# Kernel tuning notes

Hardware: AMD Instinct MI355X
Metric: run time of the kernel (lower is better)

Reference implementation:

```python
import jax, jax.numpy as jnp
import numpy as np
from jax import lax

H = 100  # hidden size (hardcoded in the module)


def _lstm_cell(x, h, c, W_ih, W_hh, b):
    # gates: [B, 4H] in PyTorch order i, f, g, o
    gates = x @ W_ih.T + h @ W_hh.T + b
    i, f, g, o = jnp.split(gates, 4, axis=-1)
    c = jax.nn.sigmoid(f) * c + jax.nn.sigmoid(i) * jnp.tanh(g)
    h = jax.nn.sigmoid(o) * jnp.tanh(c)
    return h, c


def setup_inputs() -> dict:
    key = jax.random.key(0)
    ks = jax.random.split(key, 12)
    B, T = 512, 1000
    s = 0.1  # keep gates away from saturation
    return {
        "input": jax.random.normal(ks[0], (B, T), dtype=jnp.float32),
        "W_ih1": jax.random.normal(ks[1], (4 * H, 1), dtype=jnp.float32) * s,
        "W_hh1": jax.random.normal(ks[2], (4 * H, H), dtype=jnp.float32) * s,
        "b_ih1": jax.random.normal(ks[3], (4 * H,), dtype=jnp.float32) * s,
        "b_hh1": jax.random.normal(ks[4], (4 * H,), dtype=jnp.float32) * s,
        "W_ih2": jax.random.normal(ks[5], (4 * H, H), dtype=jnp.float32) * s,
        "W_hh2": jax.random.normal(ks[6], (4 * H, H), dtype=jnp.float32) * s,
        "b_ih2": jax.random.normal(ks[7], (4 * H,), dtype=jnp.float32) * s,
        "b_hh2": jax.random.normal(ks[8], (4 * H,), dtype=jnp.float32) * s,
        "W_lin": jax.random.normal(ks[9], (1, H), dtype=jnp.float32) * s,
        "b_lin": jax.random.normal(ks[10], (1,), dtype=jnp.float32) * s,
        "future": 300,
    }


def reference(input, W_ih1, W_hh1, b_ih1, b_hh1, W_ih2, W_hh2, b_ih2, b_hh2,
              W_lin, b_lin, future):
    B = input.shape[0]
    b1 = b_ih1 + b_hh1
    b2 = b_ih2 + b_hh2
    xs = input.T[:, :, None]  # [T, B, 1]
    z = jnp.zeros((B, H), dtype=input.dtype)

    def step(carry, x):
        h1, c1, h2, c2 = carry
        h1, c1 = _lstm_cell(x, h1, c1, W_ih1, W_hh1, b1)
        h2, c2 = _lstm_cell(h1, h2, c2, W_ih2, W_hh2, b2)
        y = h2 @ W_lin.T + b_lin  # [B, 1]
        return (h1, c1, h2, c2), y

    carry, ys = lax.scan(step, (z, z, z, z), xs)  # ys: [T, B, 1]

    def fstep(carry, _):
        h1, c1, h2, c2, y = carry
        h1, c1 = _lstm_cell(y, h1, c1, W_ih1, W_hh1, b1)
        h2, c2 = _lstm_cell(h1, h2, c2, W_ih2, W_hh2, b2)
        y = h2 @ W_lin.T + b_lin
        return (h1, c1, h2, c2, y), y

    h1, c1, h2, c2 = carry
    _, ys_f = lax.scan(fstep, (h1, c1, h2, c2, ys[-1]), None, length=future)

    out = jnp.concatenate([ys, ys_f], axis=0)  # [T+future, B, 1]
    return out[:, :, 0].T  # [B, T+future]
```

## Files before the change

kernel.cpp:

```cpp
#include <hip/hip_runtime.h>
#include <stdint.h>

#define HID 100
#define B_TOTAL 512
#define T_IN 1000
#define NB 2
#define BLOCK 512
#define RSTR 160

typedef __fp16 f16x8 __attribute__((ext_vector_type(8)));
typedef __fp16 f16x2 __attribute__((ext_vector_type(2)));
typedef float f32x4 __attribute__((ext_vector_type(4)));

#define MF(A, B, C) __builtin_amdgcn_mfma_f32_16x16x32_f16((A), (B), (C), 0, 0, 0)
#define Z4 ((f32x4){0.f, 0.f, 0.f, 0.f})

#if __has_builtin(__builtin_amdgcn_exp2f)
#define EXP2F(x) __builtin_amdgcn_exp2f(x)
#else
#define EXP2F(x) exp2f(x)
#endif
#if __has_builtin(__builtin_amdgcn_rcpf)
#define RCPF(x) __builtin_amdgcn_rcpf(x)
#else
#define RCPF(x) (1.0f / (x))
#endif
#define LOG2E 1.44269504f
__device__ __forceinline__ float sigm(float x) { return RCPF(1.0f + EXP2F(-LOG2E * x)); }
__device__ __forceinline__ float tanh_fast(float x) {
  return 1.0f - 2.0f * RCPF(EXP2F((2.0f * LOG2E) * x) + 1.0f);
}

__device__ __forceinline__ float dot8(f16x8 a, f16x8 b, float acc) {
#if __has_builtin(__builtin_amdgcn_fdot2)
#pragma unroll
  for (int q = 0; q < 4; q++) {
    f16x2 xa = {a[2 * q], a[2 * q + 1]};
    f16x2 xb = {b[2 * q], b[2 * q + 1]};
    acc = __builtin_amdgcn_fdot2(xa, xb, acc, false);
  }
#else
#pragma unroll
  for (int e = 0; e < 8; e++) acc = fmaf((float)a[e], (float)b[e], acc);
#endif
  return acc;
}

__device__ __forceinline__ int jmap(int tl, int m) { return (m & 3) * 100 + 4 * tl + (m >> 2); }

__device__ __forceinline__ __fp16 w1e(const float* Whh1, const float* Wih1,
                                      const float* bih1, const float* bhh1, int j, int k) {
  if (k < 100) return (__fp16)Whh1[j * 100 + k];
  if (k == 100) return (__fp16)Wih1[j];
  if (k == 101 || k == 102) {
    float b = bih1[j] + bhh1[j];
    __fp16 hi = (__fp16)b;
    return (k == 101) ? hi : (__fp16)(b - (float)hi);
  }
  return (__fp16)0.0f;
}
__device__ __forceinline__ __fp16 w2e(const float* Wih2, const float* Whh2,
                                      const float* bih2, const float* bhh2, int j, int k) {
  if (k < 100) return (__fp16)Wih2[j * 100 + k];
  if (k == 101 || k == 102) {
    float b = bih2[j] + bhh2[j];
    __fp16 hi = (__fp16)b;
    return (k == 101) ? hi : (__fp16)(b - (float)hi);
  }
  if (k >= 112 && k < 212) return (__fp16)Whh2[j * 100 + (k - 112)];
  return (__fp16)0.0f;
}

__device__ __forceinline__ f16x8 mka1(const float* Whh1, const float* Wih1,
                                      const float* bih1, const float* bhh1,
                                      int tl, int kt, int m, int kg) {
  int j = jmap(tl, m);
  f16x8 r;
#pragma unroll
  for (int e = 0; e < 8; e++) r[e] = w1e(Whh1, Wih1, bih1, bhh1, j, kt * 32 + kg * 8 + e);
  return r;
}
__device__ __forceinline__ f16x8 mka2(const float* Wih2, const float* Whh2,
                                      const float* bih2, const float* bhh2,
                                      int tl, int kt, int m, int kg) {
  int j = jmap(tl, m);
  f16x8 r;
#pragma unroll
  for (int e = 0; e < 8; e++) r[e] = w2e(Wih2, Whh2, bih2, bhh2, j, kt * 32 + kg * 8 + e);
  return r;
}

__global__ __launch_bounds__(BLOCK, 2) void lstm2_mfma(
    const float* __restrict__ input,
    const float* __restrict__ Wih1,
    const float* __restrict__ Whh1,
    const float* __restrict__ bih1,
    const float* __restrict__ bhh1,
    const float* __restrict__ Wih2,
    const float* __restrict__ Whh2,
    const float* __restrict__ bih2,
    const float* __restrict__ bhh2,
    const float* __restrict__ Wlin,
    const float* __restrict__ blin,
    const int* __restrict__ futp,
    float* __restrict__ out)
{
  __shared__ __align__(16) __fp16 H1X[2][NB][RSTR];
  __shared__ __align__(16) __fp16 H2s[2][NB][RSTR];
  __shared__ __align__(16) float  ybuf[2][NB][104];
  __shared__ __align__(16) float  xrow[NB][T_IN];
  __shared__ __align__(16) __fp16 T24[11 * 64 * 8];
  __shared__ float wls[104];

  const int tid = threadIdx.x;
  const int lane = tid & 63;
  const int wv = tid >> 6;
  const int b0 = blockIdx.x * NB;
  const int F = futp[0];
  const int TT = T_IN + F;

  for (int i = tid; i < NB * T_IN; i += BLOCK) {
    int b = i / T_IN, tt = i % T_IN;
    xrow[b][tt] = input[(size_t)(b0 + b) * T_IN + tt];
  }
  { uint32_t* z = (uint32_t*)H1X; if (tid < 320) z[tid] = 0u; }
  { uint32_t* z = (uint32_t*)H2s; if (tid < 320) z[tid] = 0u; }
  { float* z = (float*)ybuf; if (tid < 416) z[tid] = 0.0f; }
  if (tid < 104) wls[tid] = (tid < HID) ? Wlin[tid] : 0.0f;

  const int n15 = lane & 15;
  const int kg = lane >> 4;
  const int bcol = lane & 1;

  const int sel = lane & 15;
  const int cg  = sel >> 1;
  const int ab  = sel & 1;
  const int aq  = lane >> 4;
  const int atl = (cg == 0) ? wv : (cg == 1) ? 8 + wv : (cg == 2) ? 16 + wv : 24;
  const int ak  = atl * 4 + aq;
  const bool awr1 = (sel < 6) || (wv == 0 && sel < 8);
  const bool awr2 = (sel < 6) || (wv == 1 && sel < 8);
  float c1v = 0.0f, c2v = 0.0f;

  const int is_y = (tid >= 496);
  const int ybat = ((tid - 496) >> 3) & 1;
  const int yl = (tid - 496) & 7;
  const float blin0 = blin[0];

  f16x8 wlinv[4];
#pragma unroll
  for (int i = 0; i < 4; i++) {
#pragma unroll
    for (int e = 0; e < 8; e++) {
      int k = i * 32 + kg * 8 + e;
      wlinv[i][e] = (__fp16)((k < HID) ? Wlin[k] : 0.f);
    }
  }
  f32x4 wih1q;
#pragma unroll
  for (int g = 0; g < 4; g++) wih1q[g] = Wih1[g * 100 + ak];

  f16x8 W1f0[4], W1f1[4], W1f2[4], W2f0[7], W2f1[7], W2f2[7];
#pragma unroll
  for (int kt = 0; kt < 4; kt++) {
    W1f0[kt] = mka1(Whh1, Wih1, bih1, bhh1, wv, kt, n15, kg);
    W1f1[kt] = mka1(Whh1, Wih1, bih1, bhh1, 8 + wv, kt, n15, kg);
    W1f2[kt] = mka1(Whh1, Wih1, bih1, bhh1, 16 + wv, kt, n15, kg);
  }
#pragma unroll
  for (int kt = 0; kt < 7; kt++) {
    W2f0[kt] = mka2(Wih2, Whh2, bih2, bhh2, wv, kt, n15, kg);
    W2f1[kt] = mka2(Wih2, Whh2, bih2, bhh2, 8 + wv, kt, n15, kg);
    W2f2[kt] = mka2(Wih2, Whh2, bih2, bhh2, 16 + wv, kt, n15, kg);
  }
  if (tid < 64) {
    f16x8* TV = (f16x8*)T24;
    const int m_ = tid & 15, kg_ = tid >> 4;
#pragma unroll
    for (int kt = 0; kt < 4; kt++) TV[kt * 64 + tid] = mka1(Whh1, Wih1, bih1, bhh1, 24, kt, m_, kg_);
#pragma unroll
    for (int kt = 0; kt < 3; kt++) TV[(4 + kt) * 64 + tid] = mka2(Wih2, Whh2, bih2, bhh2, 24, 4 + kt, m_, kg_);
#pragma unroll
    for (int kt = 0; kt < 4; kt++) TV[(7 + kt) * 64 + tid] = mka2(Wih2, Whh2, bih2, bhh2, 24, kt, m_, kg_);
  }

  __syncthreads();
  if (tid < 4) { H1X[tid >> 1][tid & 1][101] = (__fp16)1.0f; H1X[tid >> 1][tid & 1][102] = (__fp16)1.0f; }
  if (tid >= 4 && tid < 6) H1X[1][tid - 4][100] = (__fp16)xrow[tid - 4][0];
  __syncthreads();

  f16x8 bH1a[4], bH2[3], bl2m;
  f32x4 c0, c1, c2, c3, d0, d1, d2, d3;

#define RD_H1A(P) { _Pragma("unroll") for (int kt_ = 0; kt_ < 4; kt_++) \
    bH1a[kt_] = *(const f16x8*)&H1X[P][bcol][kt_ * 32 + kg * 8]; }
#define RD_L2M(P) { f16x8 hm_ = *(const f16x8*)&H2s[P][bcol][(kg >= 2) ? ((kg - 2) * 8) : 0]; \
    bl2m = (kg >= 2) ? hm_ : bH1a[3]; }
#define RD_H2P(P) { _Pragma("unroll") for (int kt_ = 0; kt_ < 3; kt_++) \
    bH2[kt_] = *(const f16x8*)&H2s[P][bcol][16 + kt_ * 32 + kg * 8]; }

#define MFMA_L1 { \
    c0 = Z4; c1 = Z4; c2 = Z4; c3 = Z4; \
    _Pragma("unroll") for (int kt_ = 0; kt_ < 4; kt_++) { \
      c0 = MF(W1f0[kt_], bH1a[kt_], c0); c1 = MF(W1f1[kt_], bH1a[kt_], c1); c2 = MF(W1f2[kt_], bH1a[kt_], c2); } \
    if (wv == 0) { const f16x8* TV = (const f16x8*)T24; \
      _Pragma("unroll") for (int kt_ = 0; kt_ < 4; kt_++) c3 = MF(TV[kt_ * 64 + lane], bH1a[kt_], c3); } }

#define MFMA_L2 { \
    d0 = Z4; d1 = Z4; d2 = Z4; d3 = Z4; \
    _Pragma("unroll") for (int kt_ = 0; kt_ < 3; kt_++) { \
      d0 = MF(W2f0[kt_], bH1a[kt_], d0); d1 = MF(W2f1[kt_], bH1a[kt_], d1); d2 = MF(W2f2[kt_], bH1a[kt_], d2); } \
    d0 = MF(W2f0[3], bl2m, d0); d1 = MF(W2f1[3], bl2m, d1); d2 = MF(W2f2[3], bl2m, d2); \
    _Pragma("unroll") for (int kt_ = 0; kt_ < 3; kt_++) { \
      d0 = MF(W2f0[kt_ + 4], bH2[kt_], d0); d1 = MF(W2f1[kt_ + 4], bH2[kt_], d1); d2 = MF(W2f2[kt_ + 4], bH2[kt_], d2); } \
    if (wv == 1) { const f16x8* TV = (const f16x8*)T24; \
      _Pragma("unroll") for (int kt_ = 0; kt_ < 3; kt_++) d3 = MF(TV[(7 + kt_) * 64 + lane], bH1a[kt_], d3); \
      d3 = MF(TV[10 * 64 + lane], bl2m, d3); \
      _Pragma("unroll") for (int kt_ = 0; kt_ < 3; kt_++) d3 = MF(TV[(4 + kt_) * 64 + lane], bH2[kt_], d3); } }

#define ACT1_TF(W_) { \
    f32x4 qq = (cg == 0) ? c0 : (cg == 1) ? c1 : (cg == 2) ? c2 : c3; \
    float sf_ = sigm(qq[1]), si_ = sigm(qq[0]), tg_ = tanh_fast(qq[2]); \
    c1v = sf_ * c1v + si_ * tg_; \
    float h_ = sigm(qq[3]) * tanh_fast(c1v); \
    if (awr1) H1X[W_][ab][ak] = (__fp16)h_; }

#define ACT1_AR(W_, YV_) { \
    f32x4 qq = (cg == 0) ? c0 : (cg == 1) ? c1 : (cg == 2) ? c2 : c3; \
    qq[0] = fmaf(wih1q[0], (YV_), qq[0]); qq[1] = fmaf(wih1q[1], (YV_), qq[1]); \
    qq[2] = fmaf(wih1q[2], (YV_), qq[2]); qq[3] = fmaf(wih1q[3], (YV_), qq[3]); \
    float sf_ = sigm(qq[1]), si_ = sigm(qq[0]), tg_ = tanh_fast(qq[2]); \
    c1v = sf_ * c1v + si_ * tg_; \
    float h_ = sigm(qq[3]) * tanh_fast(c1v); \
    if (awr1) H1X[W_][ab][ak] = (__fp16)h_; }

#define ACT2(W_, YB_) { \
    f32x4 qq = (cg == 0) ? d0 : (cg == 1) ? d1 : (cg == 2) ? d2 : d3; \
    float sf_ = sigm(qq[1]), si_ = sigm(qq[0]), tg_ = tanh_fast(qq[2]); \
    c2v = sf_ * c2v + si_ * tg_; \
    float h_ = sigm(qq[3]) * tanh_fast(c2v); \
    if (awr2) { H2s[W_][ab][ak] = (__fp16)h_; if (YB_) ybuf[W_][ab][ak] = h_; } }

#define Y_BODY(tt, RP) { \
    const float* yb_ = &ybuf[RP][ybat][0]; \
    float s = 0.0f; \
    _Pragma("unroll") \
    for (int m = 0; m < 13; m++) s = fmaf(yb_[yl + 8 * m], wls[yl + 8 * m], s); \
    s += __shfl_down(s, 4, 8); \
    s += __shfl_down(s, 2, 8); \
    s += __shfl_down(s, 1, 8); \
    if (yl == 0) out[(size_t)(b0 + ybat) * TT + (tt)] = s + blin0; }

  RD_H1A(1)
  MFMA_L1
  ACT1_TF(0)
  if (tid >= 80 && tid < 82) H1X[0][tid - 80][100] = (__fp16)xrow[tid - 80][1];
  __syncthreads();

  for (int t = 0; t < T_IN - 1; t++) {
    const int p = t & 1, w = p ^ 1;
    RD_H1A(p) RD_L2M(p) RD_H2P(p)
    MFMA_L2
    MFMA_L1
    if (is_y && t > 0) Y_BODY(t - 1, p)
    if (tid >= 80 && tid < 82 && t + 2 < T_IN)
      H1X[w][tid - 80][100] = (__fp16)xrow[tid - 80][t + 2];
    ACT2(w, 1)
    ACT1_TF(w)
    __syncthreads();
  }

  if (kg == 0) {
    W1f0[3][4] = (__fp16)0.f; W1f1[3][4] = (__fp16)0.f; W1f2[3][4] = (__fp16)0.f;
  }
  if (tid < 16) ((__fp16*)T24)[3 * 512 + tid * 8 + 4] = (__fp16)0.f;
  __syncthreads();

  for (int t = T_IN - 1; t < TT; t++) {
    const int p = t & 1, w = p ^ 1;
    RD_H1A(p) RD_L2M(p) RD_H2P(p)
    MFMA_L2
    MFMA_L1
    if (is_y && t == T_IN - 1) Y_BODY(t - 1, p)
    ACT2(w, 0)
    __syncthreads();
    float s_ = 0.f;
#pragma unroll
    for (int i_ = 0; i_ < 4; i_++) {
      f16x8 hh_ = *(const f16x8*)&H2s[w][bcol][i_ * 32 + kg * 8];
      s_ = dot8(hh_, wlinv[i_], s_);
    }
    s_ += __shfl_xor(s_, 16, 64);
    s_ += __shfl_xor(s_, 32, 64);
    const float yv = s_ + blin0;
    if (wv == 0 && lane < 2) out[(size_t)(b0 + lane) * TT + t] = yv;
    ACT1_AR(w, yv)
    __syncthreads();
  }
}

extern "C" void kernel_launch(void* const* d_in, const int* in_sizes, int n_in,
                              void* d_out, int out_size, void* d_ws, size_t ws_size,
                              hipStream_t stream) {
  const float* input = (const float*)d_in[0];
  const float* Wih1  = (const float*)d_in[1];
  const float* Whh1  = (const float*)d_in[2];
  const float* bih1  = (const float*)d_in[3];
  const float* bhh1  = (const float*)d_in[4];
  const float* Wih2  = (const float*)d_in[5];
  const float* Whh2  = (const float*)d_in[6];
  const float* bih2  = (const float*)d_in[7];
  const float* bhh2  = (const float*)d_in[8];
  const float* Wlin  = (const float*)d_in[9];
  const float* blin  = (const float*)d_in[10];
  const int*   futp  = (const int*)d_in[11];
  float* out = (float*)d_out;

  dim3 grid(B_TOTAL / NB);
  dim3 block(BLOCK);
  hipLaunchKernelGGL(lstm2_mfma, grid, block, 0, stream,
                     input, Wih1, Whh1, bih1, bhh1, Wih2, Whh2, bih2, bhh2,
                     Wlin, blin, futp, out);
}
```

Before: 1.576 ms.

## Halve block to four waves with all weights in registers and fused output reduction

The block shrinks from 8 waves to 4, and each wave now holds seven gate tiles of weight fragments in registers. This removes the LDS-resident T24 tile that was used for the 25th tile. The linear output projection is computed in ACT2 with a wave shuffle reduction into a small partials buffer, replacing the dedicated Y threads and the dot8 path. The aim is lower barrier cost and fewer LDS reads per step, at the price of more serial MFMA work per wave and much higher register pressure with occupancy 1.

```diff
diff --git a/kernel.cpp b/kernel.cpp
--- a/kernel.cpp
+++ b/kernel.cpp
@@ -5,15 +5,15 @@
 #define B_TOTAL 512
 #define T_IN 1000
 #define NB 2
-#define BLOCK 512
+#define BLOCK 256
 #define RSTR 160
 
 typedef __fp16 f16x8 __attribute__((ext_vector_type(8)));
-typedef __fp16 f16x2 __attribute__((ext_vector_type(2)));
 typedef float f32x4 __attribute__((ext_vector_type(4)));
 
 #define MF(A, B, C) __builtin_amdgcn_mfma_f32_16x16x32_f16((A), (B), (C), 0, 0, 0)
 #define Z4 ((f32x4){0.f, 0.f, 0.f, 0.f})
+#define ZH8 ((f16x8){(__fp16)0.f,(__fp16)0.f,(__fp16)0.f,(__fp16)0.f,(__fp16)0.f,(__fp16)0.f,(__fp16)0.f,(__fp16)0.f})
 
 #if __has_builtin(__builtin_amdgcn_exp2f)
 #define EXP2F(x) __builtin_amdgcn_exp2f(x)
@@ -31,21 +31,6 @@
   return 1.0f - 2.0f * RCPF(EXP2F((2.0f * LOG2E) * x) + 1.0f);
 }
 
-__device__ __forceinline__ float dot8(f16x8 a, f16x8 b, float acc) {
-#if __has_builtin(__builtin_amdgcn_fdot2)
-#pragma unroll
-  for (int q = 0; q < 4; q++) {
-    f16x2 xa = {a[2 * q], a[2 * q + 1]};
-    f16x2 xb = {b[2 * q], b[2 * q + 1]};
-    acc = __builtin_amdgcn_fdot2(xa, xb, acc, false);
-  }
-#else
-#pragma unroll
-  for (int e = 0; e < 8; e++) acc = fmaf((float)a[e], (float)b[e], acc);
-#endif
-  return acc;
-}
-
 __device__ __forceinline__ int jmap(int tl, int m) { return (m & 3) * 100 + 4 * tl + (m >> 2); }
 
 __device__ __forceinline__ __fp16 w1e(const float* Whh1, const float* Wih1,
@@ -90,7 +75,7 @@
   return r;
 }
 
-__global__ __launch_bounds__(BLOCK, 2) void lstm2_mfma(
+__global__ __launch_bounds__(BLOCK, 1) void lstm2_mfma(
     const float* __restrict__ input,
     const float* __restrict__ Wih1,
     const float* __restrict__ Whh1,
@@ -107,10 +92,8 @@
 {
   __shared__ __align__(16) __fp16 H1X[2][NB][RSTR];
   __shared__ __align__(16) __fp16 H2s[2][NB][RSTR];
-  __shared__ __align__(16) float  ybuf[2][NB][104];
   __shared__ __align__(16) float  xrow[NB][T_IN];
-  __shared__ __align__(16) __fp16 T24[11 * 64 * 8];
-  __shared__ float wls[104];
+  __shared__ __align__(16) float  partials[2][NB][4];
 
   const int tid = threadIdx.x;
   const int lane = tid & 63;
@@ -123,10 +106,11 @@
     int b = i / T_IN, tt = i % T_IN;
     xrow[b][tt] = input[(size_t)(b0 + b) * T_IN + tt];
   }
-  { uint32_t* z = (uint32_t*)H1X; if (tid < 320) z[tid] = 0u; }
-  { uint32_t* z = (uint32_t*)H2s; if (tid < 320) z[tid] = 0u; }
-  { float* z = (float*)ybuf; if (tid < 416) z[tid] = 0.0f; }
-  if (tid < 104) wls[tid] = (tid < HID) ? Wlin[tid] : 0.0f;
+  for (int i = tid; i < 320; i += BLOCK) {
+    ((uint32_t*)H1X)[i] = 0u;
+    ((uint32_t*)H2s)[i] = 0u;
+  }
+  if (tid < 16) ((float*)partials)[tid] = 0.0f;
 
   const int n15 = lane & 15;
   const int kg = lane >> 4;
@@ -136,52 +120,34 @@
   const int cg  = sel >> 1;
   const int ab  = sel & 1;
   const int aq  = lane >> 4;
-  const int atl = (cg == 0) ? wv : (cg == 1) ? 8 + wv : (cg == 2) ? 16 + wv : 24;
-  const int ak  = atl * 4 + aq;
-  const bool awr1 = (sel < 6) || (wv == 0 && sel < 8);
-  const bool awr2 = (sel < 6) || (wv == 1 && sel < 8);
+  const bool actv = (cg < 6) || (wv == 3 && cg == 6);
+  const int ak = actv ? ((cg == 6) ? (96 + aq) : (16 * cg + 4 * wv + aq)) : 0;
   float c1v = 0.0f, c2v = 0.0f;
-
-  const int is_y = (tid >= 496);
-  const int ybat = ((tid - 496) >> 3) & 1;
-  const int yl = (tid - 496) & 7;
   const float blin0 = blin[0];
-
-  f16x8 wlinv[4];
-#pragma unroll
-  for (int i = 0; i < 4; i++) {
-#pragma unroll
-    for (int e = 0; e < 8; e++) {
-      int k = i * 32 + kg * 8 + e;
-      wlinv[i][e] = (__fp16)((k < HID) ? Wlin[k] : 0.f);
-    }
-  }
+  const float wlsv = Wlin[ak];
   f32x4 wih1q;
 #pragma unroll
   for (int g = 0; g < 4; g++) wih1q[g] = Wih1[g * 100 + ak];
 
-  f16x8 W1f0[4], W1f1[4], W1f2[4], W2f0[7], W2f1[7], W2f2[7];
-#pragma unroll
-  for (int kt = 0; kt < 4; kt++) {
-    W1f0[kt] = mka1(Whh1, Wih1, bih1, bhh1, wv, kt, n15, kg);
-    W1f1[kt] = mka1(Whh1, Wih1, bih1, bhh1, 8 + wv, kt, n15, kg);
-    W1f2[kt] = mka1(Whh1, Wih1, bih1, bhh1, 16 + wv, kt, n15, kg);
-  }
-#pragma unroll
-  for (int kt = 0; kt < 7; kt++) {
-    W2f0[kt] = mka2(Wih2, Whh2, bih2, bhh2, wv, kt, n15, kg);
-    W2f1[kt] = mka2(Wih2, Whh2, bih2, bhh2, 8 + wv, kt, n15, kg);
-    W2f2[kt] = mka2(Wih2, Whh2, bih2, bhh2, 16 + wv, kt, n15, kg);
-  }
-  if (tid < 64) {
-    f16x8* TV = (f16x8*)T24;
-    const int m_ = tid & 15, kg_ = tid >> 4;
-#pragma unroll
-    for (int kt = 0; kt < 4; kt++) TV[kt * 64 + tid] = mka1(Whh1, Wih1, bih1, bhh1, 24, kt, m_, kg_);
-#pragma unroll
-    for (int kt = 0; kt < 3; kt++) TV[(4 + kt) * 64 + tid] = mka2(Wih2, Whh2, bih2, bhh2, 24, 4 + kt, m_, kg_);
-#pragma unroll
-    for (int kt = 0; kt < 4; kt++) TV[(7 + kt) * 64 + tid] = mka2(Wih2, Whh2, bih2, bhh2, 24, kt, m_, kg_);
+  f16x8 W1f[7][4], W2f[7][7];
+#pragma unroll
+  for (int j = 0; j < 6; j++) {
+    const int tl_ = 4 * j + wv;
+#pragma unroll
+    for (int kt = 0; kt < 4; kt++) W1f[j][kt] = mka1(Whh1, Wih1, bih1, bhh1, tl_, kt, n15, kg);
+#pragma unroll
+    for (int kt = 0; kt < 7; kt++) W2f[j][kt] = mka2(Wih2, Whh2, bih2, bhh2, tl_, kt, n15, kg);
+  }
+  if (wv == 3) {
+#pragma unroll
+    for (int kt = 0; kt < 4; kt++) W1f[6][kt] = mka1(Whh1, Wih1, bih1, bhh1, 24, kt, n15, kg);
+#pragma unroll
+    for (int kt = 0; kt < 7; kt++) W2f[6][kt] = mka2(Wih2, Whh2, bih2, bhh2, 24, kt, n15, kg);
+  } else {
+#pragma unroll
+    for (int kt = 0; kt < 4; kt++) W1f[6][kt] = ZH8;
+#pragma unroll
+    for (int kt = 0; kt < 7; kt++) W2f[6][kt] = ZH8;
   }
 
   __syncthreads();
@@ -190,7 +156,7 @@
   __syncthreads();
 
   f16x8 bH1a[4], bH2[3], bl2m;
-  f32x4 c0, c1, c2, c3, d0, d1, d2, d3;
+  f32x4 dA[7], cA[7];
 
 #define RD_H1A(P) { _Pragma("unroll") for (int kt_ = 0; kt_ < 4; kt_++) \
     bH1a[kt_] = *(const f16x8*)&H1X[P][bcol][kt_ * 32 + kg * 8]; }
@@ -199,57 +165,47 @@
 #define RD_H2P(P) { _Pragma("unroll") for (int kt_ = 0; kt_ < 3; kt_++) \
     bH2[kt_] = *(const f16x8*)&H2s[P][bcol][16 + kt_ * 32 + kg * 8]; }
 
-#define MFMA_L1 { \
-    c0 = Z4; c1 = Z4; c2 = Z4; c3 = Z4; \
-    _Pragma("unroll") for (int kt_ = 0; kt_ < 4; kt_++) { \
-      c0 = MF(W1f0[kt_], bH1a[kt_], c0); c1 = MF(W1f1[kt_], bH1a[kt_], c1); c2 = MF(W1f2[kt_], bH1a[kt_], c2); } \
-    if (wv == 0) { const f16x8* TV = (const f16x8*)T24; \
-      _Pragma("unroll") for (int kt_ = 0; kt_ < 4; kt_++) c3 = MF(TV[kt_ * 64 + lane], bH1a[kt_], c3); } }
-
-#define MFMA_L2 { \
-    d0 = Z4; d1 = Z4; d2 = Z4; d3 = Z4; \
-    _Pragma("unroll") for (int kt_ = 0; kt_ < 3; kt_++) { \
-      d0 = MF(W2f0[kt_], bH1a[kt_], d0); d1 = MF(W2f1[kt_], bH1a[kt_], d1); d2 = MF(W2f2[kt_], bH1a[kt_], d2); } \
-    d0 = MF(W2f0[3], bl2m, d0); d1 = MF(W2f1[3], bl2m, d1); d2 = MF(W2f2[3], bl2m, d2); \
-    _Pragma("unroll") for (int kt_ = 0; kt_ < 3; kt_++) { \
-      d0 = MF(W2f0[kt_ + 4], bH2[kt_], d0); d1 = MF(W2f1[kt_ + 4], bH2[kt_], d1); d2 = MF(W2f2[kt_ + 4], bH2[kt_], d2); } \
-    if (wv == 1) { const f16x8* TV = (const f16x8*)T24; \
-      _Pragma("unroll") for (int kt_ = 0; kt_ < 3; kt_++) d3 = MF(TV[(7 + kt_) * 64 + lane], bH1a[kt_], d3); \
-      d3 = MF(TV[10 * 64 + lane], bl2m, d3); \
-      _Pragma("unroll") for (int kt_ = 0; kt_ < 3; kt_++) d3 = MF(TV[(4 + kt_) * 64 + lane], bH2[kt_], d3); } }
-
-#define ACT1_TF(W_) { \
-    f32x4 qq = (cg == 0) ? c0 : (cg == 1) ? c1 : (cg == 2) ? c2 : c3; \
+#define MFMA_L2 { _Pragma("unroll") for (int j = 0; j < 7; j++) { f32x4 a_ = Z4; \
+    a_ = MF(W2f[j][0], bH1a[0], a_); a_ = MF(W2f[j][1], bH1a[1], a_); a_ = MF(W2f[j][2], bH1a[2], a_); \
+    a_ = MF(W2f[j][3], bl2m, a_); \
+    a_ = MF(W2f[j][4], bH2[0], a_); a_ = MF(W2f[j][5], bH2[1], a_); a_ = MF(W2f[j][6], bH2[2], a_); \
+    dA[j] = a_; } }
+
+#define MFMA_L1 { _Pragma("unroll") for (int j = 0; j < 7; j++) { f32x4 a_ = Z4; \
+    a_ = MF(W1f[j][0], bH1a[0], a_); a_ = MF(W1f[j][1], bH1a[1], a_); \
+    a_ = MF(W1f[j][2], bH1a[2], a_); a_ = MF(W1f[j][3], bH1a[3], a_); \
+    cA[j] = a_; } }
+
+#define SELD (cg==0?dA[0]:cg==1?dA[1]:cg==2?dA[2]:cg==3?dA[3]:cg==4?dA[4]:cg==5?dA[5]:dA[6])
+#define SELC (cg==0?cA[0]:cg==1?cA[1]:cg==2?cA[2]:cg==3?cA[3]:cg==4?cA[4]:cg==5?cA[5]:cA[6])
+
+#define ACT2(W_, PW_) { f32x4 qq = SELD; \
+    float sf_ = sigm(qq[1]), si_ = sigm(qq[0]), tg_ = tanh_fast(qq[2]); \
+    c2v = sf_ * c2v + si_ * tg_; \
+    float h_ = sigm(qq[3]) * tanh_fast(c2v); \
+    if (actv) H2s[W_][ab][ak] = (__fp16)h_; \
+    float pc_ = actv ? h_ * wlsv : 0.0f; \
+    pc_ += __shfl_xor(pc_, 2, 64);  pc_ += __shfl_xor(pc_, 4, 64); \
+    pc_ += __shfl_xor(pc_, 8, 64);  pc_ += __shfl_xor(pc_, 16, 64); \
+    pc_ += __shfl_xor(pc_, 32, 64); \
+    if (lane < 2) partials[PW_][lane][wv] = pc_; }
+
+#define ACT1_TF(W_) { f32x4 qq = SELC; \
     float sf_ = sigm(qq[1]), si_ = sigm(qq[0]), tg_ = tanh_fast(qq[2]); \
     c1v = sf_ * c1v + si_ * tg_; \
     float h_ = sigm(qq[3]) * tanh_fast(c1v); \
-    if (awr1) H1X[W_][ab][ak] = (__fp16)h_; }
-
-#define ACT1_AR(W_, YV_) { \
-    f32x4 qq = (cg == 0) ? c0 : (cg == 1) ? c1 : (cg == 2) ? c2 : c3; \
+    if (actv) H1X[W_][ab][ak] = (__fp16)h_; }
+
+#define ACT1_AR(W_, YV_) { f32x4 qq = SELC; \
     qq[0] = fmaf(wih1q[0], (YV_), qq[0]); qq[1] = fmaf(wih1q[1], (YV_), qq[1]); \
     qq[2] = fmaf(wih1q[2], (YV_), qq[2]); qq[3] = fmaf(wih1q[3], (YV_), qq[3]); \
     float sf_ = sigm(qq[1]), si_ = sigm(qq[0]), tg_ = tanh_fast(qq[2]); \
     c1v = sf_ * c1v + si_ * tg_; \
     float h_ = sigm(qq[3]) * tanh_fast(c1v); \
-    if (awr1) H1X[W_][ab][ak] = (__fp16)h_; }
-
-#define ACT2(W_, YB_) { \
-    f32x4 qq = (cg == 0) ? d0 : (cg == 1) ? d1 : (cg == 2) ? d2 : d3; \
-    float sf_ = sigm(qq[1]), si_ = sigm(qq[0]), tg_ = tanh_fast(qq[2]); \
-    c2v = sf_ * c2v + si_ * tg_; \
-    float h_ = sigm(qq[3]) * tanh_fast(c2v); \
-    if (awr2) { H2s[W_][ab][ak] = (__fp16)h_; if (YB_) ybuf[W_][ab][ak] = h_; } }
-
-#define Y_BODY(tt, RP) { \
-    const float* yb_ = &ybuf[RP][ybat][0]; \
-    float s = 0.0f; \
-    _Pragma("unroll") \
-    for (int m = 0; m < 13; m++) s = fmaf(yb_[yl + 8 * m], wls[yl + 8 * m], s); \
-    s += __shfl_down(s, 4, 8); \
-    s += __shfl_down(s, 2, 8); \
-    s += __shfl_down(s, 1, 8); \
-    if (yl == 0) out[(size_t)(b0 + ybat) * TT + (tt)] = s + blin0; }
+    if (actv) H1X[W_][ab][ak] = (__fp16)h_; }
+
+#define YSUM(PP_, DST_) { const f32x4 pv_ = *(const f32x4*)&partials[PP_][ab][0]; \
+    DST_ = pv_[0] + pv_[1] + pv_[2] + pv_[3] + blin0; }
 
   RD_H1A(1)
   MFMA_L1
@@ -261,38 +217,38 @@
     const int p = t & 1, w = p ^ 1;
     RD_H1A(p) RD_L2M(p) RD_H2P(p)
     MFMA_L2
+    ACT2(w, p)
     MFMA_L1
-    if (is_y && t > 0) Y_BODY(t - 1, p)
+    if (wv == 0 && lane < 2 && t > 0) {
+      float yv_;
+      YSUM(p ^ 1, yv_)
+      out[(size_t)(b0 + lane) * TT + (t - 1)] = yv_;
+    }
     if (tid >= 80 && tid < 82 && t + 2 < T_IN)
       H1X[w][tid - 80][100] = (__fp16)xrow[tid - 80][t + 2];
-    ACT2(w, 1)
     ACT1_TF(w)
     __syncthreads();
   }
 
   if (kg == 0) {
-    W1f0[3][4] = (__fp16)0.f; W1f1[3][4] = (__fp16)0.f; W1f2[3][4] = (__fp16)0.f;
-  }
-  if (tid < 16) ((__fp16*)T24)[3 * 512 + tid * 8 + 4] = (__fp16)0.f;
-  __syncthreads();
+#pragma unroll
+    for (int j = 0; j < 7; j++) W1f[j][3][4] = (__fp16)0.f;
+  }
 
   for (int t = T_IN - 1; t < TT; t++) {
     const int p = t & 1, w = p ^ 1;
     RD_H1A(p) RD_L2M(p) RD_H2P(p)
     MFMA_L2
+    if (t == T_IN - 1 && wv == 0 && lane < 2) {
+      float yv_;
+      YSUM(p ^ 1, yv_)
+      out[(size_t)(b0 + lane) * TT + (t - 1)] = yv_;
+    }
+    ACT2(w, p)
     MFMA_L1
-    if (is_y && t == T_IN - 1) Y_BODY(t - 1, p)
-    ACT2(w, 0)
     __syncthreads();
-    float s_ = 0.f;
-#pragma unroll
-    for (int i_ = 0; i_ < 4; i_++) {
-      f16x8 hh_ = *(const f16x8*)&H2s[w][bcol][i_ * 32 + kg * 8];
-      s_ = dot8(hh_, wlinv[i_], s_);
-    }
-    s_ += __shfl_xor(s_, 16, 64);
-    s_ += __shfl_xor(s_, 32, 64);
-    const float yv = s_ + blin0;
+    float yv;
+    YSUM(p, yv)
     if (wv == 0 && lane < 2) out[(size_t)(b0 + lane) * TT + t] = yv;
     ACT1_AR(w, yv)
     __syncthreads();
```

New measurement: 2.242 ms. 1.42x slower.

## Keep tail gate weights in registers and compute teacher-forced output via wave 7 dot

Applied to the files above, without the earlier changes.

Moves the 25th-tile weight fragments for both layers from shared memory (T24) into per-wave registers on waves 0 and 1, so the MFMA loops no longer issue LDS reads for them. The float ybuf/wls path for the linear head is replaced by wave 7 computing the output from the fp16 H2s state with packed dot8 and two shuffles. ACT2 is moved before the layer-1 MFMAs to interleave transcendental work with matrix ops. The x-input writer threads move to another wave. This raises VGPR pressure, which could spill or lower occupancy under launch_bounds(512,2), and the head now reads fp16 rather than fp32 h2 in the teacher-forced phase.

```diff
diff --git a/kernel.cpp b/kernel.cpp
--- a/kernel.cpp
+++ b/kernel.cpp
@@ -14,6 +14,7 @@
 
 #define MF(A, B, C) __builtin_amdgcn_mfma_f32_16x16x32_f16((A), (B), (C), 0, 0, 0)
 #define Z4 ((f32x4){0.f, 0.f, 0.f, 0.f})
+#define ZH8 ((f16x8){(__fp16)0.f,(__fp16)0.f,(__fp16)0.f,(__fp16)0.f,(__fp16)0.f,(__fp16)0.f,(__fp16)0.f,(__fp16)0.f})
 
 #if __has_builtin(__builtin_amdgcn_exp2f)
 #define EXP2F(x) __builtin_amdgcn_exp2f(x)
@@ -107,10 +108,7 @@
 {
   __shared__ __align__(16) __fp16 H1X[2][NB][RSTR];
   __shared__ __align__(16) __fp16 H2s[2][NB][RSTR];
-  __shared__ __align__(16) float  ybuf[2][NB][104];
   __shared__ __align__(16) float  xrow[NB][T_IN];
-  __shared__ __align__(16) __fp16 T24[11 * 64 * 8];
-  __shared__ float wls[104];
 
   const int tid = threadIdx.x;
   const int lane = tid & 63;
@@ -123,10 +121,7 @@
     int b = i / T_IN, tt = i % T_IN;
     xrow[b][tt] = input[(size_t)(b0 + b) * T_IN + tt];
   }
-  { uint32_t* z = (uint32_t*)H1X; if (tid < 320) z[tid] = 0u; }
-  { uint32_t* z = (uint32_t*)H2s; if (tid < 320) z[tid] = 0u; }
-  { float* z = (float*)ybuf; if (tid < 416) z[tid] = 0.0f; }
-  if (tid < 104) wls[tid] = (tid < HID) ? Wlin[tid] : 0.0f;
+  if (tid < 320) { ((uint32_t*)H1X)[tid] = 0u; ((uint32_t*)H2s)[tid] = 0u; }
 
   const int n15 = lane & 15;
   const int kg = lane >> 4;
@@ -141,10 +136,6 @@
   const bool awr1 = (sel < 6) || (wv == 0 && sel < 8);
   const bool awr2 = (sel < 6) || (wv == 1 && sel < 8);
   float c1v = 0.0f, c2v = 0.0f;
-
-  const int is_y = (tid >= 496);
-  const int ybat = ((tid - 496) >> 3) & 1;
-  const int yl = (tid - 496) & 7;
   const float blin0 = blin[0];
 
   f16x8 wlinv[4];
@@ -173,15 +164,18 @@
     W2f1[kt] = mka2(Wih2, Whh2, bih2, bhh2, 8 + wv, kt, n15, kg);
     W2f2[kt] = mka2(Wih2, Whh2, bih2, bhh2, 16 + wv, kt, n15, kg);
   }
-  if (tid < 64) {
-    f16x8* TV = (f16x8*)T24;
-    const int m_ = tid & 15, kg_ = tid >> 4;
-#pragma unroll
-    for (int kt = 0; kt < 4; kt++) TV[kt * 64 + tid] = mka1(Whh1, Wih1, bih1, bhh1, 24, kt, m_, kg_);
-#pragma unroll
-    for (int kt = 0; kt < 3; kt++) TV[(4 + kt) * 64 + tid] = mka2(Wih2, Whh2, bih2, bhh2, 24, 4 + kt, m_, kg_);
-#pragma unroll
-    for (int kt = 0; kt < 4; kt++) TV[(7 + kt) * 64 + tid] = mka2(Wih2, Whh2, bih2, bhh2, 24, kt, m_, kg_);
+  f16x8 W1T[4], W2T[7];
+#pragma unroll
+  for (int kt = 0; kt < 4; kt++) W1T[kt] = ZH8;
+#pragma unroll
+  for (int kt = 0; kt < 7; kt++) W2T[kt] = ZH8;
+  if (wv == 0) {
+#pragma unroll
+    for (int kt = 0; kt < 4; kt++) W1T[kt] = mka1(Whh1, Wih1, bih1, bhh1, 24, kt, n15, kg);
+  }
+  if (wv == 1) {
+#pragma unroll
+    for (int kt = 0; kt < 7; kt++) W2T[kt] = mka2(Wih2, Whh2, bih2, bhh2, 24, kt, n15, kg);
   }
 
   __syncthreads();
@@ -190,7 +184,9 @@
   __syncthreads();
 
   f16x8 bH1a[4], bH2[3], bl2m;
-  f32x4 c0, c1, c2, c3, d0, d1, d2, d3;
+  f32x4 c0, c1, c2, d0, d1, d2;
+  f32x4 c3 = Z4, d3 = Z4;
+  const f32x4 zz = Z4;
 
 #define RD_H1A(P) { _Pragma("unroll") for (int kt_ = 0; kt_ < 4; kt_++) \
     bH1a[kt_] = *(const f16x8*)&H1X[P][bcol][kt_ * 32 + kg * 8]; }
@@ -199,24 +195,27 @@
 #define RD_H2P(P) { _Pragma("unroll") for (int kt_ = 0; kt_ < 3; kt_++) \
     bH2[kt_] = *(const f16x8*)&H2s[P][bcol][16 + kt_ * 32 + kg * 8]; }
 
+#define MFMA_L2 { \
+    d0 = MF(W2f0[0], bH1a[0], zz); d1 = MF(W2f1[0], bH1a[0], zz); d2 = MF(W2f2[0], bH1a[0], zz); \
+    d0 = MF(W2f0[1], bH1a[1], d0); d1 = MF(W2f1[1], bH1a[1], d1); d2 = MF(W2f2[1], bH1a[1], d2); \
+    d0 = MF(W2f0[2], bH1a[2], d0); d1 = MF(W2f1[2], bH1a[2], d1); d2 = MF(W2f2[2], bH1a[2], d2); \
+    d0 = MF(W2f0[3], bl2m, d0);    d1 = MF(W2f1[3], bl2m, d1);    d2 = MF(W2f2[3], bl2m, d2); \
+    d0 = MF(W2f0[4], bH2[0], d0);  d1 = MF(W2f1[4], bH2[0], d1);  d2 = MF(W2f2[4], bH2[0], d2); \
+    d0 = MF(W2f0[5], bH2[1], d0);  d1 = MF(W2f1[5], bH2[1], d1);  d2 = MF(W2f2[5], bH2[1], d2); \
+    d0 = MF(W2f0[6], bH2[2], d0);  d1 = MF(W2f1[6], bH2[2], d1);  d2 = MF(W2f2[6], bH2[2], d2); \
+    if (wv == 1) { \
+      d3 = MF(W2T[0], bH1a[0], zz); d3 = MF(W2T[1], bH1a[1], d3); d3 = MF(W2T[2], bH1a[2], d3); \
+      d3 = MF(W2T[3], bl2m, d3); \
+      d3 = MF(W2T[4], bH2[0], d3);  d3 = MF(W2T[5], bH2[1], d3);  d3 = MF(W2T[6], bH2[2], d3); } }
+
 #define MFMA_L1 { \
-    c0 = Z4; c1 = Z4; c2 = Z4; c3 = Z4; \
-    _Pragma("unroll") for (int kt_ = 0; kt_ < 4; kt_++) { \
-      c0 = MF(W1f0[kt_], bH1a[kt_], c0); c1 = MF(W1f1[kt_], bH1a[kt_], c1); c2 = MF(W1f2[kt_], bH1a[kt_], c2); } \
-    if (wv == 0) { const f16x8* TV = (const f16x8*)T24; \
-      _Pragma("unroll") for (int kt_ = 0; kt_ < 4; kt_++) c3 = MF(TV[kt_ * 64 + lane], bH1a[kt_], c3); } }
-
-#define MFMA_L2 { \
-    d0 = Z4; d1 = Z4; d2 = Z4; d3 = Z4; \
-    _Pragma("unroll") for (int kt_ = 0; kt_ < 3; kt_++) { \
-      d0 = MF(W2f0[kt_], bH1a[kt_], d0); d1 = MF(W2f1[kt_], bH1a[kt_], d1); d2 = MF(W2f2[kt_], bH1a[kt_], d2); } \
-    d0 = MF(W2f0[3], bl2m, d0); d1 = MF(W2f1[3], bl2m, d1); d2 = MF(W2f2[3], bl2m, d2); \
-    _Pragma("unroll") for (int kt_ = 0; kt_ < 3; kt_++) { \
-      d0 = MF(W2f0[kt_ + 4], bH2[kt_], d0); d1 = MF(W2f1[kt_ + 4], bH2[kt_], d1); d2 = MF(W2f2[kt_ + 4], bH2[kt_], d2); } \
-    if (wv == 1) { const f16x8* TV = (const f16x8*)T24; \
-      _Pragma("unroll") for (int kt_ = 0; kt_ < 3; kt_++) d3 = MF(TV[(7 + kt_) * 64 + lane], bH1a[kt_], d3); \
-      d3 = MF(TV[10 * 64 + lane], bl2m, d3); \
-      _Pragma("unroll") for (int kt_ = 0; kt_ < 3; kt_++) d3 = MF(TV[(4 + kt_) * 64 + lane], bH2[kt_], d3); } }
+    c0 = MF(W1f0[0], bH1a[0], zz); c1 = MF(W1f1[0], bH1a[0], zz); c2 = MF(W1f2[0], bH1a[0], zz); \
+    c0 = MF(W1f0[1], bH1a[1], c0); c1 = MF(W1f1[1], bH1a[1], c1); c2 = MF(W1f2[1], bH1a[1], c2); \
+    c0 = MF(W1f0[2], bH1a[2], c0); c1 = MF(W1f1[2], bH1a[2], c1); c2 = MF(W1f2[2], bH1a[2], c2); \
+    c0 = MF(W1f0[3], bH1a[3], c0); c1 = MF(W1f1[3], bH1a[3], c1); c2 = MF(W1f2[3], bH1a[3], c2); \
+    if (wv == 0) { \
+      c3 = MF(W1T[0], bH1a[0], zz); c3 = MF(W1T[1], bH1a[1], c3); \
+      c3 = MF(W1T[2], bH1a[2], c3); c3 = MF(W1T[3], bH1a[3], c3); } }
 
 #define ACT1_TF(W_) { \
     f32x4 qq = (cg == 0) ? c0 : (cg == 1) ? c1 : (cg == 2) ? c2 : c3; \
@@ -234,55 +233,53 @@
     float h_ = sigm(qq[3]) * tanh_fast(c1v); \
     if (awr1) H1X[W_][ab][ak] = (__fp16)h_; }
 
-#define ACT2(W_, YB_) { \
+#define ACT2(W_) { \
     f32x4 qq = (cg == 0) ? d0 : (cg == 1) ? d1 : (cg == 2) ? d2 : d3; \
     float sf_ = sigm(qq[1]), si_ = sigm(qq[0]), tg_ = tanh_fast(qq[2]); \
     c2v = sf_ * c2v + si_ * tg_; \
     float h_ = sigm(qq[3]) * tanh_fast(c2v); \
-    if (awr2) { H2s[W_][ab][ak] = (__fp16)h_; if (YB_) ybuf[W_][ab][ak] = h_; } }
-
-#define Y_BODY(tt, RP) { \
-    const float* yb_ = &ybuf[RP][ybat][0]; \
-    float s = 0.0f; \
-    _Pragma("unroll") \
-    for (int m = 0; m < 13; m++) s = fmaf(yb_[yl + 8 * m], wls[yl + 8 * m], s); \
-    s += __shfl_down(s, 4, 8); \
-    s += __shfl_down(s, 2, 8); \
-    s += __shfl_down(s, 1, 8); \
-    if (yl == 0) out[(size_t)(b0 + ybat) * TT + (tt)] = s + blin0; }
+    if (awr2) H2s[W_][ab][ak] = (__fp16)h_; }
+
+#define YTF(tt, P_) { if (wv == 7) { \
+    float s_ = 0.0f; \
+    _Pragma("unroll") for (int i_ = 0; i_ < 4; i_++) { \
+      f16x8 hh_ = *(const f16x8*)&H2s[P_][bcol][i_ * 32 + kg * 8]; \
+      s_ = dot8(hh_, wlinv[i_], s_); } \
+    s_ += __shfl_xor(s_, 16, 64); \
+    s_ += __shfl_xor(s_, 32, 64); \
+    if (lane < 2) out[(size_t)(b0 + lane) * TT + (tt)] = s_ + blin0; } }
 
   RD_H1A(1)
   MFMA_L1
   ACT1_TF(0)
-  if (tid >= 80 && tid < 82) H1X[0][tid - 80][100] = (__fp16)xrow[tid - 80][1];
+  if (tid >= 384 && tid < 386) H1X[0][tid - 384][100] = (__fp16)xrow[tid - 384][1];
   __syncthreads();
 
   for (int t = 0; t < T_IN - 1; t++) {
     const int p = t & 1, w = p ^ 1;
     RD_H1A(p) RD_L2M(p) RD_H2P(p)
     MFMA_L2
+    ACT2(w)
     MFMA_L1
-    if (is_y && t > 0) Y_BODY(t - 1, p)
-    if (tid >= 80 && tid < 82 && t + 2 < T_IN)
-      H1X[w][tid - 80][100] = (__fp16)xrow[tid - 80][t + 2];
-    ACT2(w, 1)
+    if (t > 0) YTF(t - 1, p)
+    if (tid >= 384 && tid < 386 && t + 2 < T_IN)
+      H1X[w][tid - 384][100] = (__fp16)xrow[tid - 384][t + 2];
     ACT1_TF(w)
     __syncthreads();
   }
 
   if (kg == 0) {
     W1f0[3][4] = (__fp16)0.f; W1f1[3][4] = (__fp16)0.f; W1f2[3][4] = (__fp16)0.f;
-  }
-  if (tid < 16) ((__fp16*)T24)[3 * 512 + tid * 8 + 4] = (__fp16)0.f;
-  __syncthreads();
+    if (wv == 0) W1T[3][4] = (__fp16)0.f;
+  }
 
   for (int t = T_IN - 1; t < TT; t++) {
     const int p = t & 1, w = p ^ 1;
     RD_H1A(p) RD_L2M(p) RD_H2P(p)
     MFMA_L2
+    if (t == T_IN - 1) YTF(t - 1, p)
+    ACT2(w)
     MFMA_L1
-    if (is_y && t == T_IN - 1) Y_BODY(t - 1, p)
-    ACT2(w, 0)
     __syncthreads();
     float s_ = 0.f;
 #pragma unroll
```

New measurement: 1.444 ms. 8.4% less time.
